# Kernel optimization log

Measured on AMD Instinct MI355X. Metric: run time of the kernel, lower is better.

## Reference

```python
import jax, jax.numpy as jnp
import numpy as np

B, T, D, H, C = 256, 512, 300, 128, 6

def setup_inputs() -> dict:
    key = jax.random.key(0)
    ks = jax.random.split(key, 8)
    s = 1.0 / np.sqrt(H)  # PyTorch LSTM/Linear uniform init scale
    x = jax.random.normal(ks[0], (B, T, D), dtype=jnp.float32)
    lengths = jax.random.randint(ks[1], (B,), 1, T + 1)
    W_ih = jax.random.uniform(ks[2], (4 * H, D), minval=-s, maxval=s, dtype=jnp.float32)
    W_hh = jax.random.uniform(ks[3], (4 * H, H), minval=-s, maxval=s, dtype=jnp.float32)
    b_ih = jax.random.uniform(ks[4], (4 * H,), minval=-s, maxval=s, dtype=jnp.float32)
    b_hh = jax.random.uniform(ks[5], (4 * H,), minval=-s, maxval=s, dtype=jnp.float32)
    fc_w = jax.random.uniform(ks[6], (C, H), minval=-s, maxval=s, dtype=jnp.float32)
    fc_b = jax.random.uniform(ks[7], (C,), minval=-s, maxval=s, dtype=jnp.float32)
    return {"x": x, "W_ih": W_ih, "W_hh": W_hh, "b_ih": b_ih, "b_hh": b_hh,
            "fc_w": fc_w, "fc_b": fc_b, "lengths": lengths}

def _lstm_last_hidden(x, W_ih, W_hh, b_ih, b_hh, lengths):
    # Equivalent to pack_padded_sequence + nn.LSTM: the returned hidden[-1]
    # is the state at t = length-1 for each sequence. We run a masked scan:
    # state updates are frozen once t >= length.
    Bv, Tv, _ = x.shape
    Hv = W_hh.shape[1]
    xs = jnp.swapaxes(x, 0, 1)                              # [T, B, D]
    gx = jnp.einsum('tbd,gd->tbg', xs, W_ih) + b_ih + b_hh  # [T, B, 4H]
    mask = (jnp.arange(Tv)[:, None] < lengths[None, :])     # [T, B]

    def step(carry, inp):
        h, c = carry
        g, m = inp
        gates = g + h @ W_hh.T                              # [B, 4H]
        i, f, gg, o = jnp.split(gates, 4, axis=-1)          # PyTorch gate order i,f,g,o
        i = jax.nn.sigmoid(i)
        f = jax.nn.sigmoid(f)
        gg = jnp.tanh(gg)
        o = jax.nn.sigmoid(o)
        c_new = f * c + i * gg
        h_new = o * jnp.tanh(c_new)
        m = m[:, None]
        h = jnp.where(m, h_new, h)
        c = jnp.where(m, c_new, c)
        return (h, c), None

    h0 = jnp.zeros((Bv, Hv), dtype=x.dtype)
    c0 = jnp.zeros((Bv, Hv), dtype=x.dtype)
    (h, c), _ = jax.lax.scan(step, (h0, c0), (gx, mask))
    return h

def reference(x, W_ih, W_hh, b_ih, b_hh, fc_w, fc_b, lengths):
    h = _lstm_last_hidden(x, W_ih, W_hh, b_ih, b_hh, lengths)  # [B, H]
    return h @ fc_w.T + fc_b                                   # [B, 6]
```

## Files before the change

kernel.cpp:

```cpp
#include <hip/hip_runtime.h>
#include <hip/hip_bf16.h>
#include <stdint.h>
#include <type_traits>

#define NB 256
#define NT 512
#define ND 300
#define NH 128
#define NG 512
#define NC 6

typedef __attribute__((ext_vector_type(8))) short short8;
typedef __attribute__((ext_vector_type(4))) float f32x4;

static __device__ __forceinline__ float bf2f(unsigned int u) {
  return __builtin_bit_cast(float, (u & 0xffffu) << 16);
}
static __device__ __forceinline__ unsigned short f2bf(float f) {
  return __builtin_bit_cast(unsigned short, __float2bfloat16(f));
}
static __device__ __forceinline__ unsigned int packbf(float a, float b) {
  return (unsigned int)f2bf(a) | ((unsigned int)f2bf(b) << 16);
}
static __device__ __forceinline__ float ld1(const unsigned short* p) { return bf2f(*p); }
static __device__ __forceinline__ float ld1(const float* p) { return *p; }
static __device__ __forceinline__ void st1(unsigned short* p, float v) { *p = f2bf(v); }
static __device__ __forceinline__ void st1(float* p, float v) { *p = v; }

static __device__ __forceinline__ float sigmoid_fast(float x) {
  return __builtin_amdgcn_rcpf(1.f + __expf(-x));
}
static __device__ __forceinline__ float tanh_fast(float x) {
  return 1.f - 2.f * __builtin_amdgcn_rcpf(__expf(2.f * x) + 1.f);
}

static __device__ __forceinline__ uint2 load4bf_fast(const unsigned short* row, int k) {
  return *(const uint2*)(row + k);
}
static __device__ __forceinline__ uint2 load4bf_fast(const float* row, int k) {
  float4 f = *(const float4*)(row + k);
  uint2 v;
  v.x = packbf(f.x, f.y);
  v.y = packbf(f.z, f.w);
  return v;
}
static __device__ __forceinline__ uint2 load4bf(const unsigned short* row, int k, int lim) {
  if (k + 3 < lim) return load4bf_fast(row, k);
  unsigned int e0 = (k + 0 < lim) ? row[k + 0] : 0;
  unsigned int e1 = (k + 1 < lim) ? row[k + 1] : 0;
  unsigned int e2 = (k + 2 < lim) ? row[k + 2] : 0;
  unsigned int e3 = (k + 3 < lim) ? row[k + 3] : 0;
  uint2 v;
  v.x = e0 | (e1 << 16);
  v.y = e2 | (e3 << 16);
  return v;
}
static __device__ __forceinline__ uint2 load4bf(const float* row, int k, int lim) {
  if (k + 3 < lim) return load4bf_fast(row, k);
  float f0 = (k + 0 < lim) ? row[k + 0] : 0.f;
  float f1 = (k + 1 < lim) ? row[k + 1] : 0.f;
  float f2 = (k + 2 < lim) ? row[k + 2] : 0.f;
  float f3 = (k + 3 < lim) ? row[k + 3] : 0.f;
  uint2 v;
  v.x = packbf(f0, f1);
  v.y = packbf(f2, f3);
  return v;
}

__global__ void detect_dtype(const unsigned short* __restrict__ X, int* __restrict__ flag) {
  __shared__ int cnt;
  if (threadIdx.x == 0) cnt = 0;
  __syncthreads();
  int c = 0;
  for (int i = threadIdx.x; i < 512; i += 64) {
    unsigned int u = X[i];
    unsigned int e = (u >> 7) & 0xffu;
    if (u == 0u || (e >= 97u && e <= 157u)) c++;
  }
  atomicAdd(&cnt, c);
  __syncthreads();
  if (threadIdx.x == 0) *flag = (cnt >= 448) ? 0 : 1;
}

template <typename XT, typename GXT>
__global__ __launch_bounds__(256) void gx_gemm(const int* __restrict__ flag, int want,
                                               const XT* __restrict__ X,
                                               const XT* __restrict__ Wih,
                                               const XT* __restrict__ bih,
                                               const XT* __restrict__ bhh,
                                               const int* __restrict__ lengths,
                                               GXT* __restrict__ gx,
                                               int b_base, int t_base, int Tc) {
  if (*flag != want) return;
  const int mb = blockIdx.x;
  const int m0 = mb << 6;
  const int bc = m0 / Tc;
  const int trel0 = m0 % Tc;
  const int b = b_base + bc;
  const int t0 = t_base + trel0;
  const int len = lengths[b];
  if (t0 >= len) return;

  __shared__ unsigned short As[10][64][40];
  __shared__ unsigned short Bs[2][128][40];

  const int tid = threadIdx.x;
  const int lane = tid & 63;
  const int wave = tid >> 6;
  const int wm = wave & 1;
  const int wn = wave >> 1;
  const int lq = lane >> 4;
  const int lr = lane & 15;

  const int rA = tid >> 2;
  const int cA = (tid & 3) << 2;
  const XT* xrow = X + ((size_t)b * NT + t0 + rA) * ND;
  {
    uint2 a0[10], a1[10];
#pragma unroll
    for (int kc = 0; kc < 9; ++kc) {
      a0[kc] = load4bf_fast(xrow, kc * 32 + cA);
      a1[kc] = load4bf_fast(xrow, kc * 32 + 16 + cA);
    }
    a0[9] = load4bf(xrow, 288 + cA, ND);
    a1[9] = load4bf(xrow, 288 + 16 + cA, ND);
#pragma unroll
    for (int kc = 0; kc < 10; ++kc) {
      *(uint2*)&As[kc][rA][cA] = a0[kc];
      *(uint2*)&As[kc][rA][16 + cA] = a1[kc];
    }
  }

  const int rB = tid >> 1;
  const int cB = (tid & 1) << 2;

  for (int nt = 0; nt < 4; ++nt) {
    const int n0 = nt << 7;
    const XT* wrow = Wih + (size_t)(n0 + rB) * ND;

    f32x4 acc[2][4];
#pragma unroll
    for (int i = 0; i < 2; ++i)
#pragma unroll
      for (int j = 0; j < 4; ++j) {
        f32x4 z = {0.f, 0.f, 0.f, 0.f};
        acc[i][j] = z;
      }

    uint2 bv[2][4];
#pragma unroll
    for (int g4 = 0; g4 < 4; ++g4) bv[0][g4] = load4bf_fast(wrow, cB + g4 * 8);
#pragma unroll
    for (int g4 = 0; g4 < 4; ++g4) bv[1][g4] = load4bf_fast(wrow, 32 + cB + g4 * 8);

    __syncthreads();
#pragma unroll
    for (int g4 = 0; g4 < 4; ++g4) *(uint2*)&Bs[0][rB][cB + g4 * 8] = bv[0][g4];
    __syncthreads();

#pragma unroll
    for (int kc = 0; kc < 10; ++kc) {
      const int bi = kc & 1;
      if (kc < 9) {
#pragma unroll
        for (int g4 = 0; g4 < 4; ++g4)
          *(uint2*)&Bs[bi ^ 1][rB][cB + g4 * 8] = bv[bi ^ 1][g4];
      }
      if (kc < 8) {
        const int kn = (kc + 2) * 32;
        if (kc < 7) {
#pragma unroll
          for (int g4 = 0; g4 < 4; ++g4) bv[bi][g4] = load4bf_fast(wrow, kn + cB + g4 * 8);
        } else {
#pragma unroll
          for (int g4 = 0; g4 < 4; ++g4) bv[bi][g4] = load4bf(wrow, kn + cB + g4 * 8, ND);
        }
      }

      short8 af[2], bq[4];
#pragma unroll
      for (int tm = 0; tm < 2; ++tm)
        af[tm] = *(const short8*)&As[kc][wm * 32 + tm * 16 + lr][lq * 8];
#pragma unroll
      for (int tn = 0; tn < 4; ++tn)
        bq[tn] = *(const short8*)&Bs[bi][wn * 64 + tn * 16 + lr][lq * 8];
#pragma unroll
      for (int tm = 0; tm < 2; ++tm)
#pragma unroll
        for (int tn = 0; tn < 4; ++tn)
          acc[tm][tn] =
              __builtin_amdgcn_mfma_f32_16x16x32_bf16(af[tm], bq[tn], acc[tm][tn], 0, 0, 0);
      __syncthreads();
    }

    float bias_c[4];
#pragma unroll
    for (int tn = 0; tn < 4; ++tn) {
      const int col = n0 + wn * 64 + tn * 16 + lr;
      bias_c[tn] = ld1(bih + col) + ld1(bhh + col);
    }
#pragma unroll
    for (int tm = 0; tm < 2; ++tm)
#pragma unroll
      for (int tn = 0; tn < 4; ++tn)
#pragma unroll
        for (int rg = 0; rg < 4; ++rg) {
          const int row = wm * 32 + tm * 16 + lq * 4 + rg;
          if (t0 + row < len) {
            const int col = n0 + wn * 64 + tn * 16 + lr;
            st1(gx + (size_t)(m0 + row) * NG + col, acc[tm][tn][rg] + bias_c[tn]);
          }
        }
  }
}

template <typename XT, typename GXT>
__global__ __launch_bounds__(512)
__attribute__((amdgpu_waves_per_eu(2, 2)))
void lstm_rec(const int* __restrict__ flag, int want,
              const GXT* __restrict__ gx,
              const XT* __restrict__ Whh,
              const XT* __restrict__ fcw,
              const XT* __restrict__ fcb,
              const int* __restrict__ lengths,
              XT* __restrict__ out,
              float* __restrict__ hstate,
              float* __restrict__ cstate,
              int b_base, int t_base, int Tc) {
  if (*flag != want) return;
  const int bc = blockIdx.x;
  const int b = b_base + bc;
  int len = lengths[b];
  if (len > NT) len = NT;
  if (len < 0) len = 0;
  const bool first = (t_base == 0);
  const bool last = (t_base + Tc >= NT);
  const int tend = (len < t_base + Tc) ? len : (t_base + Tc);
  if (!last && tend <= t_base) return;
  int nsteps = tend - t_base;
  if (nsteps < 0) nsteps = 0;

  const int tid = threadIdx.x;
  const int w8 = tid >> 6;
  const int l = tid & 63;
  const int q = l >> 4;
  const int m = l & 15;
  const int u0 = w8 * 16 + q * 4;
  const int r = m & 3;
  const int u = u0 + r;

  __shared__ __align__(16) unsigned short hpk[2][NH];
  __shared__ __align__(16) float hf[NH];

  short8 afr[4][4];
#pragma unroll
  for (int g = 0; g < 4; ++g) {
    const int row = g * NH + w8 * 16 + m;
    if constexpr (std::is_same_v<XT, unsigned short>) {
#pragma unroll
      for (int c = 0; c < 4; ++c)
        afr[g][c] = *(const short8*)(Whh + (size_t)row * NH + c * 32 + q * 8);
    } else {
#pragma unroll
      for (int c = 0; c < 4; ++c) {
        const float* p = Whh + (size_t)row * NH + c * 32 + q * 8;
        float4 f0 = *(const float4*)p;
        float4 f1 = *(const float4*)(p + 4);
        union { unsigned int uu[4]; short8 s; } cv2;
        cv2.uu[0] = packbf(f0.x, f0.y);
        cv2.uu[1] = packbf(f0.z, f0.w);
        cv2.uu[2] = packbf(f1.x, f1.y);
        cv2.uu[3] = packbf(f1.z, f1.w);
        afr[g][c] = cv2.s;
      }
    }
  }

  float hcur = 0.f, ccur = 0.f;
  if (!first) {
    hcur = hstate[(size_t)bc * NH + u];
    ccur = cstate[(size_t)bc * NH + u];
  }
  if (m < 4) hpk[0][u] = f2bf(hcur);
  __syncthreads();

  const GXT* gp = gx + (size_t)bc * Tc * NG + u;
  const int lastidx = (nsteps > 0) ? nsteps - 1 : 0;
  float g_c[4], g_n[4];
#pragma unroll
  for (int g = 0; g < 4; ++g) {
    g_c[g] = ld1(gp + g * NH);
    g_n[g] = ld1(gp + (size_t)((1 < lastidx) ? 1 : lastidx) * NG + g * NH);
  }

  for (int s = 0; s < nsteps; ++s) {
    int idx = s + 2;
    if (idx > lastidx) idx = lastidx;
    float g_f[4];
#pragma unroll
    for (int g = 0; g < 4; ++g) g_f[g] = ld1(gp + (size_t)idx * NG + g * NH);

    short8 bfr[4];
    const unsigned short* hrow = hpk[s & 1];
#pragma unroll
    for (int c = 0; c < 4; ++c) bfr[c] = *(const short8*)&hrow[c * 32 + q * 8];

    f32x4 acc[4];
#pragma unroll
    for (int g = 0; g < 4; ++g) {
      f32x4 z = {0.f, 0.f, 0.f, 0.f};
      acc[g] = z;
#pragma unroll
      for (int c = 0; c < 4; ++c)
        acc[g] = __builtin_amdgcn_mfma_f32_16x16x32_bf16(afr[g][c], bfr[c], acc[g], 0, 0, 0);
    }

    float pre[4];
#pragma unroll
    for (int g = 0; g < 4; ++g) {
      const float t0v = (r & 1) ? acc[g][1] : acc[g][0];
      const float t1v = (r & 1) ? acc[g][3] : acc[g][2];
      pre[g] = ((r & 2) ? t1v : t0v) + g_c[g];
    }
    const float ig = sigmoid_fast(pre[0]);
    const float fg = sigmoid_fast(pre[1]);
    const float gg = tanh_fast(pre[2]);
    const float og = sigmoid_fast(pre[3]);
    ccur = fmaf(fg, ccur, ig * gg);
    hcur = og * tanh_fast(ccur);
    if (m < 4) hpk[(s + 1) & 1][u] = f2bf(hcur);
    __syncthreads();

#pragma unroll
    for (int g = 0; g < 4; ++g) {
      g_c[g] = g_n[g];
      g_n[g] = g_f[g];
    }
  }

  if (!last) {
    if (m < 4) {
      hstate[(size_t)bc * NH + u] = hcur;
      cstate[(size_t)bc * NH + u] = ccur;
    }
  } else {
    if (m < 4) hf[u] = hcur;
    __syncthreads();
    if (tid < NC) {
      float acc = ld1(fcb + tid);
      const XT* wv = fcw + (size_t)tid * NH;
#pragma unroll
      for (int k = 0; k < NH; ++k) acc = fmaf(ld1(wv + k), hf[k], acc);
      st1(out + (size_t)b * NC + tid, acc);
    }
  }
}

template <typename XT, typename GXT>
static void run_variant(int want, const int* flag, void* const* d_in, XT* out,
                        GXT* gx, float* hstate, float* cstate, int NBc, int Tc,
                        hipStream_t stream) {
  const XT* X = (const XT*)d_in[0];
  const XT* Wih = (const XT*)d_in[1];
  const XT* Whh = (const XT*)d_in[2];
  const XT* bih = (const XT*)d_in[3];
  const XT* bhh = (const XT*)d_in[4];
  const XT* fcw = (const XT*)d_in[5];
  const XT* fcb = (const XT*)d_in[6];
  const int* lengths = (const int*)d_in[7];
  for (int bb = 0; bb < NB; bb += NBc) {
    for (int tb = 0; tb < NT; tb += Tc) {
      gx_gemm<XT, GXT><<<dim3((NBc * Tc) / 64), dim3(256), 0, stream>>>(
          flag, want, X, Wih, bih, bhh, lengths, gx, bb, tb, Tc);
      lstm_rec<XT, GXT><<<dim3(NBc), dim3(512), 0, stream>>>(
          flag, want, gx, Whh, fcw, fcb, lengths, out, hstate, cstate, bb, tb, Tc);
    }
  }
}

extern "C" void kernel_launch(void* const* d_in, const int* in_sizes, int n_in,
                              void* d_out, int out_size, void* d_ws, size_t ws_size,
                              hipStream_t stream) {
  int* flag = (int*)d_ws;
  detect_dtype<<<dim3(1), dim3(64), 0, stream>>>((const unsigned short*)d_in[0], flag);

  const size_t full_f32 = (size_t)NB * NT * NG * sizeof(float);
  const size_t full_bf16 = (size_t)NB * NT * NG * 2;
  const size_t base = 512;

  int NBc, Tc;
  char* gx_raw;
  float* hstate = (float*)((char*)d_ws + base);
  bool gx_is_f32;

  if (ws_size >= base + full_f32) {
    NBc = NB; Tc = NT; gx_is_f32 = true;
    gx_raw = (char*)d_ws + base;
  } else if (ws_size >= base + full_bf16) {
    NBc = NB; Tc = NT; gx_is_f32 = false;
    gx_raw = (char*)d_ws + base;
  } else {
    Tc = 128; gx_is_f32 = false;
    NBc = 1;
    for (int cand : {64, 16, 4}) {
      size_t need = base + (size_t)cand * NH * 2 * sizeof(float) + (size_t)cand * Tc * NG * 2;
      if (ws_size >= need) { NBc = cand; break; }
    }
    gx_raw = (char*)d_ws + base + (size_t)NBc * NH * 2 * sizeof(float);
  }
  float* cstate = hstate + (size_t)NBc * NH;

  if (gx_is_f32) {
    run_variant<unsigned short, float>(0, flag, d_in, (unsigned short*)d_out,
                                       (float*)gx_raw, hstate, cstate, NBc, Tc, stream);
    run_variant<float, float>(1, flag, d_in, (float*)d_out, (float*)gx_raw, hstate,
                              cstate, NBc, Tc, stream);
  } else {
    run_variant<unsigned short, unsigned short>(0, flag, d_in, (unsigned short*)d_out,
                                                (unsigned short*)gx_raw, hstate, cstate,
                                                NBc, Tc, stream);
    run_variant<float, unsigned short>(1, flag, d_in, (float*)d_out,
                                       (unsigned short*)gx_raw, hstate, cstate, NBc, Tc,
                                       stream);
  }
}
```

Baseline: 617.2 us.

## Triple-buffer W_ih prefetch, use LDS-only barriers, unroll recurrence by two

In the input-projection GEMM, W_ih staging moves to a three-deep register prefetch with a new thread mapping, and the next n-tile's first K-chunks are loaded before the current tile's epilogue. __syncthreads is replaced by a raw s_waitcnt lgkmcnt(0) + s_barrier so barriers do not wait on outstanding global loads. The recurrence loop is unrolled by two with fixed buffer parity, which removes the rotating gx register copies and issues the gx prefetch later in each step. The raw barrier depends on the code never needing vmcnt ordering across it, which is a correctness risk if any global-to-LDS dependency exists.

```diff
diff --git a/kernel.cpp b/kernel.cpp
--- a/kernel.cpp
+++ b/kernel.cpp
@@ -33,6 +33,8 @@
 static __device__ __forceinline__ float tanh_fast(float x) {
   return 1.f - 2.f * __builtin_amdgcn_rcpf(__expf(2.f * x) + 1.f);
 }
+
+#define BARRIER_LGKM() asm volatile("s_waitcnt lgkmcnt(0)\n\ts_barrier" ::: "memory")
 
 static __device__ __forceinline__ uint2 load4bf_fast(const unsigned short* row, int k) {
   return *(const uint2*)(row + k);
@@ -131,12 +133,22 @@
     }
   }
 
-  const int rB = tid >> 1;
-  const int cB = (tid & 1) << 2;
+  const int rb = tid >> 3;
+  const int kq = tid & 7;
+
+  uint2 bv[3][4];
+  {
+    const XT* wb = Wih + (size_t)rb * ND;
+#pragma unroll
+    for (int s3 = 0; s3 < 3; ++s3)
+#pragma unroll
+      for (int j = 0; j < 4; ++j)
+        bv[s3][j] = load4bf_fast(wb + (size_t)(32 * j) * ND, s3 * 32 + kq * 4);
+  }
 
   for (int nt = 0; nt < 4; ++nt) {
     const int n0 = nt << 7;
-    const XT* wrow = Wih + (size_t)(n0 + rB) * ND;
+    const XT* wb = Wih + (size_t)(n0 + rb) * ND;
 
     f32x4 acc[2][4];
 #pragma unroll
@@ -147,33 +159,28 @@
         acc[i][j] = z;
       }
 
-    uint2 bv[2][4];
-#pragma unroll
-    for (int g4 = 0; g4 < 4; ++g4) bv[0][g4] = load4bf_fast(wrow, cB + g4 * 8);
-#pragma unroll
-    for (int g4 = 0; g4 < 4; ++g4) bv[1][g4] = load4bf_fast(wrow, 32 + cB + g4 * 8);
-
-    __syncthreads();
-#pragma unroll
-    for (int g4 = 0; g4 < 4; ++g4) *(uint2*)&Bs[0][rB][cB + g4 * 8] = bv[0][g4];
-    __syncthreads();
+#pragma unroll
+    for (int j = 0; j < 4; ++j) *(uint2*)&Bs[0][rb + 32 * j][kq * 4] = bv[0][j];
+    BARRIER_LGKM();
 
 #pragma unroll
     for (int kc = 0; kc < 10; ++kc) {
       const int bi = kc & 1;
       if (kc < 9) {
 #pragma unroll
-        for (int g4 = 0; g4 < 4; ++g4)
-          *(uint2*)&Bs[bi ^ 1][rB][cB + g4 * 8] = bv[bi ^ 1][g4];
+        for (int j = 0; j < 4; ++j)
+          *(uint2*)&Bs[bi ^ 1][rb + 32 * j][kq * 4] = bv[(kc + 1) % 3][j];
       }
-      if (kc < 8) {
-        const int kn = (kc + 2) * 32;
-        if (kc < 7) {
-#pragma unroll
-          for (int g4 = 0; g4 < 4; ++g4) bv[bi][g4] = load4bf_fast(wrow, kn + cB + g4 * 8);
+      if (kc < 7) {
+        const int kn = (kc + 3) * 32 + kq * 4;
+        if (kc < 6) {
+#pragma unroll
+          for (int j = 0; j < 4; ++j)
+            bv[kc % 3][j] = load4bf_fast(wb + (size_t)(32 * j) * ND, kn);
         } else {
 #pragma unroll
-          for (int g4 = 0; g4 < 4; ++g4) bv[bi][g4] = load4bf(wrow, kn + cB + g4 * 8, ND);
+          for (int j = 0; j < 4; ++j)
+            bv[kc % 3][j] = load4bf(wb + (size_t)(32 * j) * ND, kn, ND);
         }
       }
 
@@ -190,7 +197,16 @@
         for (int tn = 0; tn < 4; ++tn)
           acc[tm][tn] =
               __builtin_amdgcn_mfma_f32_16x16x32_bf16(af[tm], bq[tn], acc[tm][tn], 0, 0, 0);
-      __syncthreads();
+      BARRIER_LGKM();
+    }
+
+    if (nt < 3) {
+      const XT* wb2 = Wih + (size_t)((nt + 1) * 128 + rb) * ND;
+#pragma unroll
+      for (int s3 = 0; s3 < 3; ++s3)
+#pragma unroll
+        for (int j = 0; j < 4; ++j)
+          bv[s3][j] = load4bf_fast(wb2 + (size_t)(32 * j) * ND, s3 * 32 + kq * 4);
     }
 
     float bias_c[4];
@@ -286,57 +302,62 @@
 
   const GXT* gp = gx + (size_t)bc * Tc * NG + u;
   const int lastidx = (nsteps > 0) ? nsteps - 1 : 0;
-  float g_c[4], g_n[4];
-#pragma unroll
-  for (int g = 0; g < 4; ++g) {
-    g_c[g] = ld1(gp + g * NH);
-    g_n[g] = ld1(gp + (size_t)((1 < lastidx) ? 1 : lastidx) * NG + g * NH);
-  }
-
-  for (int s = 0; s < nsteps; ++s) {
-    int idx = s + 2;
-    if (idx > lastidx) idx = lastidx;
-    float g_f[4];
-#pragma unroll
-    for (int g = 0; g < 4; ++g) g_f[g] = ld1(gp + (size_t)idx * NG + g * NH);
-
-    short8 bfr[4];
-    const unsigned short* hrow = hpk[s & 1];
-#pragma unroll
-    for (int c = 0; c < 4; ++c) bfr[c] = *(const short8*)&hrow[c * 32 + q * 8];
-
-    f32x4 acc[4];
+
+  float gs0[4], gs1[4];
+  {
+    const int i1 = (1 < lastidx) ? 1 : lastidx;
 #pragma unroll
     for (int g = 0; g < 4; ++g) {
-      f32x4 z = {0.f, 0.f, 0.f, 0.f};
-      acc[g] = z;
-#pragma unroll
-      for (int c = 0; c < 4; ++c)
-        acc[g] = __builtin_amdgcn_mfma_f32_16x16x32_bf16(afr[g][c], bfr[c], acc[g], 0, 0, 0);
-    }
-
-    float pre[4];
-#pragma unroll
-    for (int g = 0; g < 4; ++g) {
-      const float t0v = (r & 1) ? acc[g][1] : acc[g][0];
-      const float t1v = (r & 1) ? acc[g][3] : acc[g][2];
-      pre[g] = ((r & 2) ? t1v : t0v) + g_c[g];
-    }
-    const float ig = sigmoid_fast(pre[0]);
-    const float fg = sigmoid_fast(pre[1]);
-    const float gg = tanh_fast(pre[2]);
-    const float og = sigmoid_fast(pre[3]);
-    ccur = fmaf(fg, ccur, ig * gg);
-    hcur = og * tanh_fast(ccur);
-    if (m < 4) hpk[(s + 1) & 1][u] = f2bf(hcur);
-    __syncthreads();
-
-#pragma unroll
-    for (int g = 0; g < 4; ++g) {
-      g_c[g] = g_n[g];
-      g_n[g] = g_f[g];
-    }
-  }
+      gs0[g] = ld1(gp + g * NH);
+      gs1[g] = ld1(gp + (size_t)i1 * NG + g * NH);
+    }
+  }
+
+#define REC_STEP(S, PAR, GC)                                                         \
+  {                                                                                  \
+    short8 bfr[4];                                                                   \
+    const unsigned short* hrow = hpk[(PAR)];                                         \
+    _Pragma("unroll") for (int c = 0; c < 4; ++c)                                    \
+        bfr[c] = *(const short8*)&hrow[c * 32 + q * 8];                              \
+    f32x4 acc[4];                                                                    \
+    _Pragma("unroll") for (int g = 0; g < 4; ++g) {                                  \
+      f32x4 z = {0.f, 0.f, 0.f, 0.f};                                                \
+      acc[g] = z;                                                                    \
+      _Pragma("unroll") for (int c = 0; c < 4; ++c)                                  \
+          acc[g] = __builtin_amdgcn_mfma_f32_16x16x32_bf16(afr[g][c], bfr[c],        \
+                                                           acc[g], 0, 0, 0);         \
+    }                                                                                \
+    float pre[4];                                                                    \
+    _Pragma("unroll") for (int g = 0; g < 4; ++g) {                                  \
+      const float t0v = (r & 1) ? acc[g][1] : acc[g][0];                             \
+      const float t1v = (r & 1) ? acc[g][3] : acc[g][2];                             \
+      pre[g] = ((r & 2) ? t1v : t0v) + GC[g];                                        \
+    }                                                                                \
+    {                                                                                \
+      int idx_ = (S) + 2;                                                            \
+      if (idx_ > lastidx) idx_ = lastidx;                                            \
+      _Pragma("unroll") for (int g = 0; g < 4; ++g)                                  \
+          GC[g] = ld1(gp + (size_t)idx_ * NG + g * NH);                              \
+    }                                                                                \
+    const float ig = sigmoid_fast(pre[0]);                                           \
+    const float fg = sigmoid_fast(pre[1]);                                           \
+    const float gg = tanh_fast(pre[2]);                                              \
+    const float og = sigmoid_fast(pre[3]);                                           \
+    ccur = fmaf(fg, ccur, ig * gg);                                                  \
+    hcur = og * tanh_fast(ccur);                                                     \
+    if (m < 4) hpk[(PAR) ^ 1][u] = f2bf(hcur);                                       \
+    BARRIER_LGKM();                                                                  \
+  }
+
+  int s = 0;
+  for (; s + 1 < nsteps; s += 2) {
+    REC_STEP(s, 0, gs0);
+    REC_STEP(s + 1, 1, gs1);
+  }
+  if (s < nsteps) {
+    REC_STEP(s, 0, gs0);
+  }
+#undef REC_STEP
 
   if (!last) {
     if (m < 4) {
```

New measurement: 583.8 us. -5.4%, faster.
